# Optimization experiments

Hardware: AMD Instinct MI355X
Metric: run time of the kernel (lower is better)

Reference implementation:

```python
import jax, jax.numpy as jnp
import numpy as np

H = 768
F = 3072
NH = 12
EPS = 1e-5


def _layer_norm(x, g, b):
    mu = jnp.mean(x, axis=-1, keepdims=True)
    var = jnp.mean(jnp.square(x - mu), axis=-1, keepdims=True)
    return (x - mu) * jax.lax.rsqrt(var + EPS) * g + b


def setup_inputs() -> dict:
    key = jax.random.key(0)
    ks = jax.random.split(key, 16)
    s = 0.02
    d = {
        'x': jax.random.normal(ks[0], (2, 2048, H), jnp.float32),
        'Wq': jax.random.normal(ks[1], (H, H), jnp.float32) * s,
        'bq': jnp.zeros((H,), jnp.float32),
        'Wk': jax.random.normal(ks[2], (H, H), jnp.float32) * s,
        'bk': jnp.zeros((H,), jnp.float32),
        'Wv': jax.random.normal(ks[3], (H, H), jnp.float32) * s,
        'bv': jnp.zeros((H,), jnp.float32),
        'Wa1': jax.random.normal(ks[4], (H, H), jnp.float32) * s,
        'ba1': jnp.zeros((H,), jnp.float32),
        'g1': jnp.ones((H,), jnp.float32),
        'be1': jnp.zeros((H,), jnp.float32),
        'W1': jax.random.normal(ks[5], (H, F), jnp.float32) * s,
        'b1': jnp.zeros((F,), jnp.float32),
        'W2': jax.random.normal(ks[6], (F, H), jnp.float32) * s,
        'b2': jnp.zeros((H,), jnp.float32),
        'Wa2': jax.random.normal(ks[7], (H, H), jnp.float32) * s,
        'ba2': jnp.zeros((H,), jnp.float32),
        'g2': jnp.ones((H,), jnp.float32),
        'be2': jnp.zeros((H,), jnp.float32),
    }
    return d


def reference(x, Wq, bq, Wk, bk, Wv, bv, Wa1, ba1, g1, be1, W1, b1, W2, b2, Wa2, ba2, g2, be2):
    B, S, _ = x.shape
    Dh = H // NH
    # multi-head attention (naive: explicit scores + softmax)
    q = (x @ Wq + bq).reshape(B, S, NH, Dh)
    k = (x @ Wk + bk).reshape(B, S, NH, Dh)
    v = (x @ Wv + bv).reshape(B, S, NH, Dh)
    scores = jnp.einsum('bqhd,bkhd->bhqk', q, k) / jnp.sqrt(jnp.float32(Dh))
    att = jax.nn.softmax(scores, axis=-1)
    ctx = jnp.einsum('bhqk,bkhd->bqhd', att, v).reshape(B, S, H)
    # add_norm_1: Linear -> LayerNorm, then residual added AFTER LN (as in source)
    an1 = _layer_norm(ctx @ Wa1 + ba1, g1, be1) + x
    # feed-forward with exact GELU (torch nn.GELU default)
    ff = jax.nn.gelu(an1 @ W1 + b1, approximate=False) @ W2 + b2
    # add_norm_2: Linear -> LayerNorm, residual after LN
    out = _layer_norm(ff @ Wa2 + ba2, g2, be2) + an1
    return out
```

## Files before the change

### kernel.cpp

```cpp
#include <hip/hip_runtime.h>
#include <stdint.h>
#include <stddef.h>

#define HD 768
#define FF 3072
#define NHEAD 12
#define DHEAD 64
#define SEQ 2048
#define BATCH 2
#define NTOK (SEQ*BATCH)
#define SM_SCALE 0.18033688f

typedef __attribute__((ext_vector_type(8))) __bf16 bf16x8;
typedef __attribute__((ext_vector_type(4))) float f32x4;

__device__ __forceinline__ unsigned short f2bf(float f) {
  unsigned int u = __builtin_bit_cast(unsigned int, f);
  u += 0x7fffu + ((u >> 16) & 1u);
  return (unsigned short)(u >> 16);
}
__device__ __forceinline__ float bf2f(unsigned int s) {
  unsigned int u = s << 16;
  return __builtin_bit_cast(float, u);
}
__device__ __forceinline__ float4 ld4bf(const unsigned short* p) {
  uint2 w = *reinterpret_cast<const uint2*>(p);
  float4 o;
  o.x = bf2f(w.x & 0xffffu); o.y = bf2f(w.x >> 16);
  o.z = bf2f(w.y & 0xffffu); o.w = bf2f(w.y >> 16);
  return o;
}

__device__ __forceinline__ void gl16(const unsigned short* g, unsigned short* l) {
  __builtin_amdgcn_global_load_lds(
      (const __attribute__((address_space(1))) void*)g,
      (__attribute__((address_space(3))) void*)l,
      16, 0, 0);
}

__global__ void k_prep(const float* __restrict__ Wq, const float* __restrict__ Wk,
                       const float* __restrict__ Wv, const float* __restrict__ Wa1,
                       const float* __restrict__ W1, const float* __restrict__ W2,
                       const float* __restrict__ Wa2,
                       unsigned short* __restrict__ WqkvT, unsigned short* __restrict__ Wa1T,
                       unsigned short* __restrict__ W1T, unsigned short* __restrict__ W2T,
                       unsigned short* __restrict__ Wa2T,
                       const float* __restrict__ x, unsigned short* __restrict__ xb, int n4,
                       const float* __restrict__ bq, const float* __restrict__ bk,
                       const float* __restrict__ bv, float* __restrict__ biasqkv) {
  int t = blockIdx.x;
  int tid = threadIdx.x;
  if (t >= 7488) {
    int tb = t - 7488;
    if (tb < 9) {
      int idx = tb * 256 + tid;
      if (idx < 3*HD) {
        float v = idx < HD ? bq[idx] : idx < 2*HD ? bk[idx-HD] : bv[idx-2*HD];
        biasqkv[idx] = v;
      }
    }
    int i = tb * 256 + tid;
    int stride = 2048 * 256;
    for (; i < n4; i += stride) {
      float4 v = reinterpret_cast<const float4*>(x)[i];
      ushort4 o;
      o.x = f2bf(v.x); o.y = f2bf(v.y); o.z = f2bf(v.z); o.w = f2bf(v.w);
      reinterpret_cast<ushort4*>(xb)[i] = o;
    }
    return;
  }
  __shared__ float tile[32][33];
  const float* in; unsigned short* out; int K, N;
  if (t < 2304)      { int seg = t / 576; t -= seg * 576; K = HD; N = HD;
                       in  = seg==0 ? Wq : seg==1 ? Wk : seg==2 ? Wv : Wa1;
                       out = seg<3 ? WqkvT + seg*HD*HD : Wa1T; }
  else if (t < 4608) { t -= 2304; in = W1;  out = W1T;  K = HD; N = FF; }
  else if (t < 6912) { t -= 4608; in = W2;  out = W2T;  K = FF; N = HD; }
  else               { t -= 6912; in = Wa2; out = Wa2T; K = HD; N = HD; }
  int nt = N / 32;
  int nb = (t % nt) * 32, kb = (t / nt) * 32;
  int tx = tid & 31, ty = tid >> 5;
  for (int i = ty; i < 32; i += 8)
    tile[i][tx] = in[(size_t)(kb + i) * N + nb + tx];
  __syncthreads();
  for (int i = ty; i < 32; i += 8)
    out[(size_t)(nb + i) * K + kb + tx] = f2bf(tile[tx][i]);
}


#define BN 128
#define BK 64

template<int MODE, int TBM>
__global__ __launch_bounds__(256, 3)
void k_gemm(const unsigned short* __restrict__ A, const unsigned short* __restrict__ Bt,
            const float* __restrict__ bias, void* __restrict__ Cout,
            unsigned short* __restrict__ Vout,
            int M, int N, int K) {
  constexpr int MR = TBM / 32;
  constexpr int AI = TBM / 32;
  __shared__ unsigned short As[TBM*BK];
  __shared__ unsigned short Bs[BN*BK];
  int tid = threadIdx.x;
  int nwg = gridDim.x * gridDim.y;
  int lin = blockIdx.x + gridDim.x * blockIdx.y;
  int nl = (lin & 7) * (nwg >> 3) + (lin >> 3);
  int bm = (nl % gridDim.x) * TBM;
  int bn = (nl / gridDim.x) * BN;
  int wave = tid >> 6, lane = tid & 63;
  int wm = wave >> 1, wn = wave & 1;
  int wr = wm * (TBM/2);
  int wc = wn * 64;
  int fr = lane & 15;
  int hi = lane >> 4;

  f32x4 acc[MR][4];
#pragma unroll
  for (int m = 0; m < MR; ++m)
#pragma unroll
    for (int n = 0; n < 4; ++n) acc[m][n] = (f32x4){0.f,0.f,0.f,0.f};

  int g8 = lane >> 3;
  int cc = (lane & 7) ^ g8;
  int arow = (TBM/4)*wave + g8;
  int brow = 32*wave + g8;
  const unsigned short* ag = A + (size_t)(bm + arow) * K + cc*8;
  const unsigned short* bg = Bt + (size_t)(bn + brow) * K + cc*8;
  unsigned short* asl = As + (TBM/4)*wave*BK;
  unsigned short* bsl = Bs + 32*wave*BK;

  for (int k0 = 0; k0 < K; k0 += BK) {
#pragma unroll
    for (int i = 0; i < AI; ++i)
      gl16(ag + (size_t)(8*i)*K + k0, asl + (8*i)*BK);
#pragma unroll
    for (int i = 0; i < 4; ++i)
      gl16(bg + (size_t)(8*i)*K + k0, bsl + (8*i)*BK);
    __syncthreads();

    bf16x8 af[MR][2], bf[4][2];
#pragma unroll
    for (int m = 0; m < MR; ++m) {
      int R = wr + m*16 + fr, sw = R & 7;
#pragma unroll
      for (int h2 = 0; h2 < 2; ++h2)
        af[m][h2] = __builtin_bit_cast(bf16x8,
          *reinterpret_cast<const uint4*>(&As[R*BK + ((hi + h2*4) ^ sw)*8]));
    }
#pragma unroll
    for (int n = 0; n < 4; ++n) {
      int R = wc + n*16 + fr, sw = R & 7;
#pragma unroll
      for (int h2 = 0; h2 < 2; ++h2)
        bf[n][h2] = __builtin_bit_cast(bf16x8,
          *reinterpret_cast<const uint4*>(&Bs[R*BK + ((hi + h2*4) ^ sw)*8]));
    }
#pragma unroll
    for (int m = 0; m < MR; ++m)
#pragma unroll
      for (int n = 0; n < 4; ++n) {
        acc[m][n] = __builtin_amdgcn_mfma_f32_16x16x32_bf16(af[m][0], bf[n][0], acc[m][n], 0, 0, 0);
        acc[m][n] = __builtin_amdgcn_mfma_f32_16x16x32_bf16(af[m][1], bf[n][1], acc[m][n], 0, 0, 0);
      }
    __syncthreads();
  }

  int crow0 = (lane >> 4) * 4;
  int ccol = lane & 15;

  if (MODE == 3 && bn >= 2*HD) {
    unsigned short* tb = (wave < 2) ? As + wave*4096 : Bs + (wave-2)*4096;
#pragma unroll
    for (int m = 0; m < MR; ++m)
#pragma unroll
      for (int n = 0; n < 4; ++n)
#pragma unroll
        for (int r = 0; r < 4; ++r) {
          int tl = m*16 + crow0 + r;
          int cl = n*16 + ccol;
          float v = acc[m][n][r] + bias[bn + wc + cl];
          int pt = ((tl>>2)&3)*16 + ((tl>>4)<<2) + (tl&3);
          tb[cl*64 + (((pt>>3) ^ (cl&7))<<3) + (pt&7)] = f2bf(v);
        }
    __syncthreads();
    int tk0 = bm + wr;
    int bb = tk0 >> 11;
    int sb = tk0 & 2047;
    int hh = (bn + wc - 2*HD) >> 6;
    unsigned short* dst = Vout + ((size_t)(bb*NHEAD + hh) * DHEAD) * SEQ + sb;
#pragma unroll
    for (int p = 0; p < 8; ++p) {
      int dr = p*8 + (lane >> 3);
      int cj = lane & 7;
      uint4 w = *reinterpret_cast<const uint4*>(&tb[dr*64 + ((cj ^ (dr&7))<<3)]);
      *reinterpret_cast<uint4*>(dst + (size_t)dr*SEQ + cj*8) = w;
    }
    return;
  }

#pragma unroll
  for (int m = 0; m < MR; ++m) {
#pragma unroll
    for (int n = 0; n < 4; ++n) {
      int gcol = bn + wc + n*16 + ccol;
      float bv_ = bias[gcol];
#pragma unroll
      for (int r = 0; r < 4; ++r) {
        int grow = bm + wr + m*16 + crow0 + r;
        float v = acc[m][n][r] + bv_;
        if (MODE == 2) {
          float a = v + 0.044715f * v * v * v;
          v = v / (1.0f + exp2f(-2.3022082f * a));
        }
        if (MODE == 3 && gcol < HD) v *= SM_SCALE;
        reinterpret_cast<unsigned short*>(Cout)[(size_t)grow * N + gcol] = f2bf(v);
      }
    }
  }
}


#define KVB 64
#define KP 72

__global__ __launch_bounds__(256, 3)
void k_attn_mfma(const unsigned short* __restrict__ qkv,
                 const unsigned short* __restrict__ vt,
                 unsigned short* __restrict__ ctx) {
  __shared__ unsigned short Ks[KVB][KP];
  __shared__ unsigned short Vt[DHEAD][KP];
  __shared__ f32x4 Mg[2][9][64];

  int tid = threadIdx.x;
  int wv = tid >> 6, lane = tid & 63;
  int lo = lane & 15, hi = lane >> 4;
  int qh = wv & 1;
  int kh = wv >> 1;

  int lin = blockIdx.x + 32*(blockIdx.y + NHEAD*blockIdx.z);
  int nl = (lin & 7) * 96 + (lin >> 3);
  int qb = nl & 31;
  int rest = nl >> 5;
  int h = rest % NHEAD;
  int b = rest / NHEAD;
  int q0 = qb * 64;

  const unsigned short* qpA = qkv + (size_t)(b*SEQ + q0 + qh*32 + lo) * 2304 + h*DHEAD + hi*8;
  const unsigned short* qpB = qpA + (size_t)16 * 2304;
  bf16x8 qfA0 = __builtin_bit_cast(bf16x8, *reinterpret_cast<const uint4*>(qpA));
  bf16x8 qfA1 = __builtin_bit_cast(bf16x8, *reinterpret_cast<const uint4*>(qpA + 32));
  bf16x8 qfB0 = __builtin_bit_cast(bf16x8, *reinterpret_cast<const uint4*>(qpB));
  bf16x8 qfB1 = __builtin_bit_cast(bf16x8, *reinterpret_cast<const uint4*>(qpB + 32));

  f32x4 poA[4], poB[4];
#pragma unroll
  for (int dt = 0; dt < 4; ++dt) { poA[dt] = (f32x4){0.f,0.f,0.f,0.f}; poB[dt] = (f32x4){0.f,0.f,0.f,0.f}; }
  float lrA = 0.f, lrB = 0.f;

  int sr = tid >> 2, scg = (tid & 3) * 16;
  const unsigned short* kgl = qkv + (size_t)(b*SEQ)*2304 + HD + h*DHEAD;
  const unsigned short* vgl = vt + ((size_t)(b*NHEAD + h)) * DHEAD * SEQ;

  for (int t0 = 0; t0 < SEQ; t0 += KVB) {
    const unsigned short* kp = kgl + (size_t)(t0 + sr)*2304 + scg;
    const unsigned short* vp = vgl + (size_t)sr*SEQ + t0 + scg;
    uint4 ku0 = *reinterpret_cast<const uint4*>(kp);
    uint4 ku1 = *reinterpret_cast<const uint4*>(kp + 8);
    uint4 vu0 = *reinterpret_cast<const uint4*>(vp);
    uint4 vu1 = *reinterpret_cast<const uint4*>(vp + 8);
    __syncthreads();
    *reinterpret_cast<uint4*>(&Ks[sr][scg])     = ku0;
    *reinterpret_cast<uint4*>(&Ks[sr][scg + 8]) = ku1;
    *reinterpret_cast<uint4*>(&Vt[sr][scg])     = vu0;
    *reinterpret_cast<uint4*>(&Vt[sr][scg + 8]) = vu1;
    __syncthreads();

    f32x4 sA[2], sB[2];
#pragma unroll
    for (int kg = 0; kg < 2; ++kg) {
      int krow = kh*32 + kg*16 + lo;
      bf16x8 a0 = __builtin_bit_cast(bf16x8, *reinterpret_cast<const uint4*>(&Ks[krow][hi*8]));
      bf16x8 a1 = __builtin_bit_cast(bf16x8, *reinterpret_cast<const uint4*>(&Ks[krow][32 + hi*8]));
      f32x4 s = (f32x4){0.f,0.f,0.f,0.f};
      s = __builtin_amdgcn_mfma_f32_16x16x32_bf16(a0, qfA0, s, 0, 0, 0);
      s = __builtin_amdgcn_mfma_f32_16x16x32_bf16(a1, qfA1, s, 0, 0, 0);
      sA[kg] = s;
      s = (f32x4){0.f,0.f,0.f,0.f};
      s = __builtin_amdgcn_mfma_f32_16x16x32_bf16(a0, qfB0, s, 0, 0, 0);
      s = __builtin_amdgcn_mfma_f32_16x16x32_bf16(a1, qfB1, s, 0, 0, 0);
      sB[kg] = s;
    }

    unsigned int pwA[4], pwB[4];
#pragma unroll
    for (int kg = 0; kg < 2; ++kg) {
      float a0 = exp2f(sA[kg][0]), a1 = exp2f(sA[kg][1]);
      float a2 = exp2f(sA[kg][2]), a3 = exp2f(sA[kg][3]);
      lrA += a0 + a1 + a2 + a3;
      asm("v_cvt_pk_bf16_f32 %0, %1, %2" : "=v"(pwA[kg*2])   : "v"(a0), "v"(a1));
      asm("v_cvt_pk_bf16_f32 %0, %1, %2" : "=v"(pwA[kg*2+1]) : "v"(a2), "v"(a3));
      float b0 = exp2f(sB[kg][0]), b1 = exp2f(sB[kg][1]);
      float b2 = exp2f(sB[kg][2]), b3 = exp2f(sB[kg][3]);
      lrB += b0 + b1 + b2 + b3;
      asm("v_cvt_pk_bf16_f32 %0, %1, %2" : "=v"(pwB[kg*2])   : "v"(b0), "v"(b1));
      asm("v_cvt_pk_bf16_f32 %0, %1, %2" : "=v"(pwB[kg*2+1]) : "v"(b2), "v"(b3));
    }

    uint4 uA; uA.x = pwA[0]; uA.y = pwA[1]; uA.z = pwA[2]; uA.w = pwA[3];
    uint4 uB; uB.x = pwB[0]; uB.y = pwB[1]; uB.z = pwB[2]; uB.w = pwB[3];
    bf16x8 paA = __builtin_bit_cast(bf16x8, uA);
    bf16x8 paB = __builtin_bit_cast(bf16x8, uB);

#pragma unroll
    for (int dt = 0; dt < 4; ++dt) {
      int col = dt*16 + lo;
      bf16x8 vv = __builtin_bit_cast(bf16x8, *reinterpret_cast<const uint4*>(&Vt[col][hi*16 + kh*8]));
      poA[dt] = __builtin_amdgcn_mfma_f32_16x16x32_bf16(paA, vv, poA[dt], 0, 0, 0);
      poB[dt] = __builtin_amdgcn_mfma_f32_16x16x32_bf16(paB, vv, poB[dt], 0, 0, 0);
    }
  }

  if (kh == 1) {
#pragma unroll
    for (int dt = 0; dt < 4; ++dt) {
      Mg[qh][dt][lane] = poA[dt];
      Mg[qh][4 + dt][lane] = poB[dt];
    }
    Mg[qh][8][lane] = (f32x4){lrA, lrB, 0.f, 0.f};
  }
  __syncthreads();
  if (kh == 0) {
#pragma unroll
    for (int dt = 0; dt < 4; ++dt) {
      f32x4 mA = Mg[qh][dt][lane], mB = Mg[qh][4 + dt][lane];
      poA[dt][0] += mA[0]; poA[dt][1] += mA[1]; poA[dt][2] += mA[2]; poA[dt][3] += mA[3];
      poB[dt][0] += mB[0]; poB[dt][1] += mB[1]; poB[dt][2] += mB[2]; poB[dt][3] += mB[3];
    }
    f32x4 lm = Mg[qh][8][lane];
    lrA += lm[0]; lrB += lm[1];
    lrA += __shfl_xor(lrA, 16); lrA += __shfl_xor(lrA, 32);
    lrB += __shfl_xor(lrB, 16); lrB += __shfl_xor(lrB, 32);

    unsigned short* op = ctx + (size_t)(b*SEQ + q0 + qh*32) * HD + h*DHEAD;
#pragma unroll
    for (int r = 0; r < 4; ++r) {
      float LA = __shfl(lrA, hi*4 + r);
      float LB = __shfl(lrB, hi*4 + r);
      float liA = (LA > 0.f) ? 1.0f / LA : 0.f;
      float liB = (LB > 0.f) ? 1.0f / LB : 0.f;
      int row = hi*4 + r;
#pragma unroll
      for (int dt = 0; dt < 4; ++dt) {
        op[(size_t)row*HD + dt*16 + lo]        = f2bf(poA[dt][r] * liA);
        op[(size_t)(16 + row)*HD + dt*16 + lo] = f2bf(poB[dt][r] * liB);
      }
    }
  }
}

template<int RESID_BF16, int WRITE_F32>
__global__ __launch_bounds__(256, 4)
void k_ln(const unsigned short* __restrict__ xin, const void* __restrict__ resid_,
          const float* __restrict__ g, const float* __restrict__ be,
          float* __restrict__ outf, unsigned short* __restrict__ outb) {
  int wave = threadIdx.x >> 6, lane = threadIdx.x & 63;
  int row = blockIdx.x * 4 + wave;
  const unsigned short* xp = xin + (size_t)row * HD;
  const float4* gp = reinterpret_cast<const float4*>(g);
  const float4* bp = reinterpret_cast<const float4*>(be);
  float4 v[3];
  float sum = 0.f, sq = 0.f;
#pragma unroll
  for (int i = 0; i < 3; ++i) {
    v[i] = ld4bf(xp + (lane + 64*i)*4);
    sum += v[i].x + v[i].y + v[i].z + v[i].w;
    sq  += v[i].x*v[i].x + v[i].y*v[i].y + v[i].z*v[i].z + v[i].w*v[i].w;
  }
#pragma unroll
  for (int m = 1; m < 64; m <<= 1) { sum += __shfl_xor(sum, m); sq += __shfl_xor(sq, m); }
  float mean = sum * (1.0f/768.0f);
  float var = sq * (1.0f/768.0f) - mean*mean;
  float rstd = rsqrtf(var + 1e-5f);
#pragma unroll
  for (int i = 0; i < 3; ++i) {
    float4 gg = gp[lane + 64*i], bb = bp[lane + 64*i];
    float4 rr;
    if (RESID_BF16)
      rr = ld4bf((const unsigned short*)resid_ + (size_t)row * HD + (lane + 64*i)*4);
    else
      rr = reinterpret_cast<const float4*>((const float*)resid_ + (size_t)row * HD)[lane + 64*i];
    float4 o;
    o.x = (v[i].x - mean)*rstd*gg.x + bb.x + rr.x;
    o.y = (v[i].y - mean)*rstd*gg.y + bb.y + rr.y;
    o.z = (v[i].z - mean)*rstd*gg.z + bb.z + rr.z;
    o.w = (v[i].w - mean)*rstd*gg.w + bb.w + rr.w;
    if (WRITE_F32) {
      reinterpret_cast<float4*>(outf + (size_t)row * HD)[lane + 64*i] = o;
    } else {
      ushort4 ob;
      ob.x = f2bf(o.x); ob.y = f2bf(o.y); ob.z = f2bf(o.z); ob.w = f2bf(o.w);
      reinterpret_cast<ushort4*>(outb + (size_t)row * HD)[lane + 64*i] = ob;
    }
  }
}


extern "C" void kernel_launch(void* const* d_in, const int* in_sizes, int n_in,
                              void* d_out, int out_size, void* d_ws, size_t ws_size,
                              hipStream_t stream) {
  const float* x   = (const float*)d_in[0];
  const float* Wq  = (const float*)d_in[1];
  const float* bq  = (const float*)d_in[2];
  const float* Wk  = (const float*)d_in[3];
  const float* bk  = (const float*)d_in[4];
  const float* Wv  = (const float*)d_in[5];
  const float* bv  = (const float*)d_in[6];
  const float* Wa1 = (const float*)d_in[7];
  const float* ba1 = (const float*)d_in[8];
  const float* g1  = (const float*)d_in[9];
  const float* be1 = (const float*)d_in[10];
  const float* W1  = (const float*)d_in[11];
  const float* b1  = (const float*)d_in[12];
  const float* W2  = (const float*)d_in[13];
  const float* b2  = (const float*)d_in[14];
  const float* Wa2 = (const float*)d_in[15];
  const float* ba2 = (const float*)d_in[16];
  const float* g2  = (const float*)d_in[17];
  const float* be2 = (const float*)d_in[18];

  char* ws = (char*)d_ws;
  size_t off = 0;
  auto alloc = [&](size_t bytes) -> void* {
    void* p = ws + off;
    off += (bytes + 255) & ~(size_t)255;
    return p;
  };
  unsigned short* xb    = (unsigned short*)alloc((size_t)NTOK*HD*2);
  unsigned short* WqkvT = (unsigned short*)alloc((size_t)3*HD*HD*2);
  unsigned short* Wa1T  = (unsigned short*)alloc((size_t)HD*HD*2);
  unsigned short* W1T   = (unsigned short*)alloc((size_t)FF*HD*2);
  unsigned short* W2T   = (unsigned short*)alloc((size_t)HD*FF*2);
  unsigned short* Wa2T  = (unsigned short*)alloc((size_t)HD*HD*2);
  float*          biasqkv = (float*)alloc((size_t)3*HD*4);
  unsigned short* qkvb  = (unsigned short*)alloc((size_t)NTOK*3*HD*2);
  unsigned short* vtb   = (unsigned short*)alloc((size_t)NTOK*HD*2);
  unsigned short* ctxb  = (unsigned short*)alloc((size_t)NTOK*HD*2);
  unsigned short* a1b   = (unsigned short*)alloc((size_t)NTOK*HD*2);
  unsigned short* an1b  = (unsigned short*)alloc((size_t)NTOK*HD*2);
  unsigned short* h1g   = (unsigned short*)alloc((size_t)NTOK*FF*2);
  unsigned short* f2b   = (unsigned short*)alloc((size_t)NTOK*HD*2);
  unsigned short* a2b   = (unsigned short*)alloc((size_t)NTOK*HD*2);
  (void)ws_size; (void)in_sizes; (void)n_in; (void)out_size;

  k_prep<<<9536, 256, 0, stream>>>(Wq, Wk, Wv, Wa1, W1, W2, Wa2,
                                   WqkvT, Wa1T, W1T, W2T, Wa2T,
                                   x, xb, NTOK*HD/4, bq, bk, bv, biasqkv);

  k_gemm<3,128><<<dim3(NTOK/128, 2304/BN), 256, 0, stream>>>(xb, WqkvT, biasqkv, qkvb, vtb, NTOK, 3*HD, HD);
  k_attn_mfma<<<dim3(SEQ/64, NHEAD, BATCH), 256, 0, stream>>>(qkvb, vtb, ctxb);
  k_gemm<1,64><<<dim3(NTOK/64, HD/BN), 256, 0, stream>>>(ctxb, Wa1T, ba1, a1b, nullptr, NTOK, HD, HD);
  k_ln<0,0><<<NTOK/4, 256, 0, stream>>>(a1b, x, g1, be1, nullptr, an1b);
  k_gemm<2,128><<<dim3(NTOK/128, FF/BN), 256, 0, stream>>>(an1b, W1T, b1, h1g, nullptr, NTOK, FF, HD);
  k_gemm<1,64><<<dim3(NTOK/64, HD/BN), 256, 0, stream>>>(h1g, W2T, b2, f2b, nullptr, NTOK, HD, FF);
  k_gemm<1,64><<<dim3(NTOK/64, HD/BN), 256, 0, stream>>>(f2b, Wa2T, ba2, a2b, nullptr, NTOK, HD, HD);
  k_ln<1,1><<<NTOK/4, 256, 0, stream>>>(a2b, an1b, g2, be2, (float*)d_out, nullptr);
}
```

Measured before the change: 192.4 us.

## Double attention KV tile to 128 and compute row sums via ones-column MFMA

```diff
diff --git a/kernel.cpp b/kernel.cpp
--- a/kernel.cpp
+++ b/kernel.cpp
@@ -220,16 +220,18 @@
 }
 
 
-#define KVB 64
-#define KP 72
+#define KVB 128
+#define KPK 72
+#define KPV 136
 
 __global__ __launch_bounds__(256, 3)
 void k_attn_mfma(const unsigned short* __restrict__ qkv,
                  const unsigned short* __restrict__ vt,
                  unsigned short* __restrict__ ctx) {
-  __shared__ unsigned short Ks[KVB][KP];
-  __shared__ unsigned short Vt[DHEAD][KP];
-  __shared__ f32x4 Mg[2][9][64];
+  __shared__ __align__(16) char smem[40960];
+  auto Ks = reinterpret_cast<unsigned short(*)[KPK]>(smem);
+  auto Vt = reinterpret_cast<unsigned short(*)[KPV]>(smem + 18432);
+  auto Mg = reinterpret_cast<f32x4(*)[64]>(smem);
 
   int tid = threadIdx.x;
   int wv = tid >> 6, lane = tid & 63;
@@ -245,6 +247,11 @@
   int b = rest / NHEAD;
   int q0 = qb * 64;
 
+  for (int idx = tid; idx < 16*KPV; idx += 256) {
+    int rr = idx / KPV, cc2 = idx - rr*KPV;
+    Vt[64 + rr][cc2] = (rr == 0) ? (unsigned short)0x3F80 : (unsigned short)0;
+  }
+
   const unsigned short* qpA = qkv + (size_t)(b*SEQ + q0 + qh*32 + lo) * 2304 + h*DHEAD + hi*8;
   const unsigned short* qpB = qpA + (size_t)16 * 2304;
   bf16x8 qfA0 = __builtin_bit_cast(bf16x8, *reinterpret_cast<const uint4*>(qpA));
@@ -252,33 +259,43 @@
   bf16x8 qfB0 = __builtin_bit_cast(bf16x8, *reinterpret_cast<const uint4*>(qpB));
   bf16x8 qfB1 = __builtin_bit_cast(bf16x8, *reinterpret_cast<const uint4*>(qpB + 32));
 
-  f32x4 poA[4], poB[4];
+  f32x4 poA[4], poB[4], po5A, po5B;
 #pragma unroll
   for (int dt = 0; dt < 4; ++dt) { poA[dt] = (f32x4){0.f,0.f,0.f,0.f}; poB[dt] = (f32x4){0.f,0.f,0.f,0.f}; }
-  float lrA = 0.f, lrB = 0.f;
-
-  int sr = tid >> 2, scg = (tid & 3) * 16;
+  po5A = (f32x4){0.f,0.f,0.f,0.f};
+  po5B = (f32x4){0.f,0.f,0.f,0.f};
+
+  int ksr = tid >> 1, kc = (tid & 1) * 32;
+  int vdr = tid >> 2, vc = (tid & 3) * 32;
   const unsigned short* kgl = qkv + (size_t)(b*SEQ)*2304 + HD + h*DHEAD;
   const unsigned short* vgl = vt + ((size_t)(b*NHEAD + h)) * DHEAD * SEQ;
 
   for (int t0 = 0; t0 < SEQ; t0 += KVB) {
-    const unsigned short* kp = kgl + (size_t)(t0 + sr)*2304 + scg;
-    const unsigned short* vp = vgl + (size_t)sr*SEQ + t0 + scg;
+    const unsigned short* kp = kgl + (size_t)(t0 + ksr)*2304 + kc;
+    const unsigned short* vp = vgl + (size_t)vdr*SEQ + t0 + vc;
     uint4 ku0 = *reinterpret_cast<const uint4*>(kp);
     uint4 ku1 = *reinterpret_cast<const uint4*>(kp + 8);
+    uint4 ku2 = *reinterpret_cast<const uint4*>(kp + 16);
+    uint4 ku3 = *reinterpret_cast<const uint4*>(kp + 24);
     uint4 vu0 = *reinterpret_cast<const uint4*>(vp);
     uint4 vu1 = *reinterpret_cast<const uint4*>(vp + 8);
+    uint4 vu2 = *reinterpret_cast<const uint4*>(vp + 16);
+    uint4 vu3 = *reinterpret_cast<const uint4*>(vp + 24);
     __syncthreads();
-    *reinterpret_cast<uint4*>(&Ks[sr][scg])     = ku0;
-    *reinterpret_cast<uint4*>(&Ks[sr][scg + 8]) = ku1;
-    *reinterpret_cast<uint4*>(&Vt[sr][scg])     = vu0;
-    *reinterpret_cast<uint4*>(&Vt[sr][scg + 8]) = vu1;
+    *reinterpret_cast<uint4*>(&Ks[ksr][kc])      = ku0;
+    *reinterpret_cast<uint4*>(&Ks[ksr][kc + 8])  = ku1;
+    *reinterpret_cast<uint4*>(&Ks[ksr][kc + 16]) = ku2;
+    *reinterpret_cast<uint4*>(&Ks[ksr][kc + 24]) = ku3;
+    *reinterpret_cast<uint4*>(&Vt[vdr][vc])      = vu0;
+    *reinterpret_cast<uint4*>(&Vt[vdr][vc + 8])  = vu1;
+    *reinterpret_cast<uint4*>(&Vt[vdr][vc + 16]) = vu2;
+    *reinterpret_cast<uint4*>(&Vt[vdr][vc + 24]) = vu3;
     __syncthreads();
 
-    f32x4 sA[2], sB[2];
-#pragma unroll
-    for (int kg = 0; kg < 2; ++kg) {
-      int krow = kh*32 + kg*16 + lo;
+    f32x4 sA[4], sB[4];
+#pragma unroll
+    for (int kg = 0; kg < 4; ++kg) {
+      int krow = kh*64 + kg*16 + lo;
       bf16x8 a0 = __builtin_bit_cast(bf16x8, *reinterpret_cast<const uint4*>(&Ks[krow][hi*8]));
       bf16x8 a1 = __builtin_bit_cast(bf16x8, *reinterpret_cast<const uint4*>(&Ks[krow][32 + hi*8]));
       f32x4 s = (f32x4){0.f,0.f,0.f,0.f};
@@ -291,61 +308,75 @@
       sB[kg] = s;
     }
 
-    unsigned int pwA[4], pwB[4];
-#pragma unroll
-    for (int kg = 0; kg < 2; ++kg) {
+    unsigned int pwA[8], pwB[8];
+#pragma unroll
+    for (int kg = 0; kg < 4; ++kg) {
       float a0 = exp2f(sA[kg][0]), a1 = exp2f(sA[kg][1]);
       float a2 = exp2f(sA[kg][2]), a3 = exp2f(sA[kg][3]);
-      lrA += a0 + a1 + a2 + a3;
       asm("v_cvt_pk_bf16_f32 %0, %1, %2" : "=v"(pwA[kg*2])   : "v"(a0), "v"(a1));
       asm("v_cvt_pk_bf16_f32 %0, %1, %2" : "=v"(pwA[kg*2+1]) : "v"(a2), "v"(a3));
       float b0 = exp2f(sB[kg][0]), b1 = exp2f(sB[kg][1]);
       float b2 = exp2f(sB[kg][2]), b3 = exp2f(sB[kg][3]);
-      lrB += b0 + b1 + b2 + b3;
       asm("v_cvt_pk_bf16_f32 %0, %1, %2" : "=v"(pwB[kg*2])   : "v"(b0), "v"(b1));
       asm("v_cvt_pk_bf16_f32 %0, %1, %2" : "=v"(pwB[kg*2+1]) : "v"(b2), "v"(b3));
     }
 
-    uint4 uA; uA.x = pwA[0]; uA.y = pwA[1]; uA.z = pwA[2]; uA.w = pwA[3];
-    uint4 uB; uB.x = pwB[0]; uB.y = pwB[1]; uB.z = pwB[2]; uB.w = pwB[3];
-    bf16x8 paA = __builtin_bit_cast(bf16x8, uA);
-    bf16x8 paB = __builtin_bit_cast(bf16x8, uB);
+    uint4 uA0; uA0.x = pwA[0]; uA0.y = pwA[1]; uA0.z = pwA[2]; uA0.w = pwA[3];
+    uint4 uA1; uA1.x = pwA[4]; uA1.y = pwA[5]; uA1.z = pwA[6]; uA1.w = pwA[7];
+    uint4 uB0; uB0.x = pwB[0]; uB0.y = pwB[1]; uB0.z = pwB[2]; uB0.w = pwB[3];
+    uint4 uB1; uB1.x = pwB[4]; uB1.y = pwB[5]; uB1.z = pwB[6]; uB1.w = pwB[7];
+    bf16x8 paA0 = __builtin_bit_cast(bf16x8, uA0);
+    bf16x8 paA1 = __builtin_bit_cast(bf16x8, uA1);
+    bf16x8 paB0 = __builtin_bit_cast(bf16x8, uB0);
+    bf16x8 paB1 = __builtin_bit_cast(bf16x8, uB1);
 
 #pragma unroll
     for (int dt = 0; dt < 4; ++dt) {
       int col = dt*16 + lo;
-      bf16x8 vv = __builtin_bit_cast(bf16x8, *reinterpret_cast<const uint4*>(&Vt[col][hi*16 + kh*8]));
-      poA[dt] = __builtin_amdgcn_mfma_f32_16x16x32_bf16(paA, vv, poA[dt], 0, 0, 0);
-      poB[dt] = __builtin_amdgcn_mfma_f32_16x16x32_bf16(paB, vv, poB[dt], 0, 0, 0);
-    }
-  }
-
+      bf16x8 v0 = __builtin_bit_cast(bf16x8, *reinterpret_cast<const uint4*>(&Vt[col][kh*64 + hi*16]));
+      bf16x8 v1 = __builtin_bit_cast(bf16x8, *reinterpret_cast<const uint4*>(&Vt[col][kh*64 + hi*16 + 8]));
+      poA[dt] = __builtin_amdgcn_mfma_f32_16x16x32_bf16(paA0, v0, poA[dt], 0, 0, 0);
+      poA[dt] = __builtin_amdgcn_mfma_f32_16x16x32_bf16(paA1, v1, poA[dt], 0, 0, 0);
+      poB[dt] = __builtin_amdgcn_mfma_f32_16x16x32_bf16(paB0, v0, poB[dt], 0, 0, 0);
+      poB[dt] = __builtin_amdgcn_mfma_f32_16x16x32_bf16(paB1, v1, poB[dt], 0, 0, 0);
+    }
+    {
+      bf16x8 o0 = __builtin_bit_cast(bf16x8, *reinterpret_cast<const uint4*>(&Vt[64 + lo][kh*64 + hi*16]));
+      bf16x8 o1 = __builtin_bit_cast(bf16x8, *reinterpret_cast<const uint4*>(&Vt[64 + lo][kh*64 + hi*16 + 8]));
+      po5A = __builtin_amdgcn_mfma_f32_16x16x32_bf16(paA0, o0, po5A, 0, 0, 0);
+      po5A = __builtin_amdgcn_mfma_f32_16x16x32_bf16(paA1, o1, po5A, 0, 0, 0);
+      po5B = __builtin_amdgcn_mfma_f32_16x16x32_bf16(paB0, o0, po5B, 0, 0, 0);
+      po5B = __builtin_amdgcn_mfma_f32_16x16x32_bf16(paB1, o1, po5B, 0, 0, 0);
+    }
+  }
+
+  __syncthreads();
   if (kh == 1) {
 #pragma unroll
     for (int dt = 0; dt < 4; ++dt) {
-      Mg[qh][dt][lane] = poA[dt];
-      Mg[qh][4 + dt][lane] = poB[dt];
-    }
-    Mg[qh][8][lane] = (f32x4){lrA, lrB, 0.f, 0.f};
+      Mg[qh*10 + dt][lane] = poA[dt];
+      Mg[qh*10 + 4 + dt][lane] = poB[dt];
+    }
+    Mg[qh*10 + 8][lane] = po5A;
+    Mg[qh*10 + 9][lane] = po5B;
   }
   __syncthreads();
   if (kh == 0) {
 #pragma unroll
     for (int dt = 0; dt < 4; ++dt) {
-      f32x4 mA = Mg[qh][dt][lane], mB = Mg[qh][4 + dt][lane];
+      f32x4 mA = Mg[qh*10 + dt][lane], mB = Mg[qh*10 + 4 + dt][lane];
       poA[dt][0] += mA[0]; poA[dt][1] += mA[1]; poA[dt][2] += mA[2]; poA[dt][3] += mA[3];
       poB[dt][0] += mB[0]; poB[dt][1] += mB[1]; poB[dt][2] += mB[2]; poB[dt][3] += mB[3];
     }
-    f32x4 lm = Mg[qh][8][lane];
-    lrA += lm[0]; lrB += lm[1];
-    lrA += __shfl_xor(lrA, 16); lrA += __shfl_xor(lrA, 32);
-    lrB += __shfl_xor(lrB, 16); lrB += __shfl_xor(lrB, 32);
+    f32x4 m5A = Mg[qh*10 + 8][lane], m5B = Mg[qh*10 + 9][lane];
+    po5A[0] += m5A[0]; po5A[1] += m5A[1]; po5A[2] += m5A[2]; po5A[3] += m5A[3];
+    po5B[0] += m5B[0]; po5B[1] += m5B[1]; po5B[2] += m5B[2]; po5B[3] += m5B[3];
 
     unsigned short* op = ctx + (size_t)(b*SEQ + q0 + qh*32) * HD + h*DHEAD;
 #pragma unroll
     for (int r = 0; r < 4; ++r) {
-      float LA = __shfl(lrA, hi*4 + r);
-      float LB = __shfl(lrB, hi*4 + r);
+      float LA = __shfl(po5A[r], hi*16);
+      float LB = __shfl(po5B[r], hi*16);
       float liA = (LA > 0.f) ? 1.0f / LA : 0.f;
       float liB = (LB > 0.f) ? 1.0f / LB : 0.f;
       int row = hi*4 + r;
```

New measurement: 189.9 us. Within noise of the previous version (-1.3%).
